# Kernel tuning notes

Measured on AMD Instinct MI355X. Metric: run time of the kernel, lower is better.

Reference implementation:

```python
import jax, jax.numpy as jnp
import numpy as np

N, IN_DIM, HIDDEN, OUT_DIM = 16384, 4, 64, 2


def setup_inputs() -> dict:
    key = jax.random.key(0)
    ks = jax.random.split(key, 12)
    x = jax.random.normal(ks[0], (N, IN_DIM), dtype=jnp.float32)
    adj = jax.random.uniform(ks[1], (N, N), dtype=jnp.float32)
    adj = adj / jnp.sum(adj, axis=1, keepdims=True)  # row-normalised
    s = 0.1
    return {
        "x": x,
        "adj": adj,
        # msg_mlp: Linear(4,64) -> Tanh -> Linear(64,64)
        "W1": jax.random.normal(ks[2], (IN_DIM, HIDDEN), dtype=jnp.float32) * s,
        "b1": jnp.zeros((HIDDEN,), dtype=jnp.float32),
        "W2": jax.random.normal(ks[3], (HIDDEN, HIDDEN), dtype=jnp.float32) * s,
        "b2": jnp.zeros((HIDDEN,), dtype=jnp.float32),
        # update_mlp: Linear(68,64) -> Tanh -> Linear(64,64) -> Tanh
        "U1": jax.random.normal(ks[4], (IN_DIM + HIDDEN, HIDDEN), dtype=jnp.float32) * s,
        "c1": jnp.zeros((HIDDEN,), dtype=jnp.float32),
        "U2": jax.random.normal(ks[5], (HIDDEN, HIDDEN), dtype=jnp.float32) * s,
        "c2": jnp.zeros((HIDDEN,), dtype=jnp.float32),
        # out_head: Linear(64,2)
        "Wo": jax.random.normal(ks[6], (HIDDEN, OUT_DIM), dtype=jnp.float32) * s,
        "bo": jnp.zeros((OUT_DIM,), dtype=jnp.float32),
    }


def reference(x, adj, W1, b1, W2, b2, U1, c1, U2, c2, Wo, bo):
    # messages = msg_mlp(x): (N, HIDDEN)
    messages = jnp.tanh(x @ W1 + b1) @ W2 + b2
    # aggregate over neighbours: (N,N) @ (N,HIDDEN)
    agg = adj @ messages
    # combined = [x, agg]: (N, IN_DIM+HIDDEN)
    combined = jnp.concatenate([x, agg], axis=-1)
    h = jnp.tanh(jnp.tanh(combined @ U1 + c1) @ U2 + c2)
    acc = h @ Wo + bo  # (N, OUT_DIM)
    return acc
```

## Files before the change

### kernel.cpp

```cpp
#include <hip/hip_runtime.h>
#include <math.h>

#define NN 16384
#define IN_DIM 4
#define HID 64
#define OUT_DIM 2
#define SPLITS 4
#define KCH (NN / SPLITS)

typedef __bf16 bf16x8 __attribute__((ext_vector_type(8)));
typedef float  f32x4  __attribute__((ext_vector_type(4)));

__global__ __launch_bounds__(256) void k_messages(
    const float* __restrict__ x, const float* __restrict__ W1,
    const float* __restrict__ b1, const float* __restrict__ W2,
    const float* __restrict__ b2, __bf16* __restrict__ msgT)
{
    __shared__ float  xs[64 * 4];
    __shared__ float  h1[64 * 64];
    __shared__ __bf16 mt[64 * 66];

    const int t = threadIdx.x;
    const int node0 = blockIdx.x * 64;
    xs[t] = x[node0 * 4 + t];
    __syncthreads();

    const int h = t & 63, g = t >> 6;
    for (int n = g * 16; n < g * 16 + 16; ++n) {
        float acc = b1[h];
        #pragma unroll
        for (int k = 0; k < 4; ++k) acc += xs[n * 4 + k] * W1[k * 64 + h];
        h1[n * 64 + h] = tanhf(acc);
    }
    __syncthreads();
    for (int n = g * 16; n < g * 16 + 16; ++n) {
        float acc = b2[h];
        #pragma unroll 8
        for (int k = 0; k < 64; ++k) acc += h1[n * 64 + k] * W2[k * 64 + h];
        mt[h * 66 + n] = (__bf16)acc;
    }
    __syncthreads();
    for (int slot = t; slot < 512; slot += 256) {
        const int r = slot >> 3, c = (slot & 7) * 8;
        bf16x8 v;
        #pragma unroll
        for (int j = 0; j < 8; ++j) v[j] = mt[r * 66 + c + j];
        *(bf16x8*)(msgT + (size_t)r * NN + node0 + c) = v;
    }
}

__global__ __launch_bounds__(256) void k_agg(
    const float* __restrict__ adj, const __bf16* __restrict__ msgT,
    float* __restrict__ part)
{
    const int t = threadIdx.x;
    const int wave = t >> 6, lane = t & 63;
    const int s = blockIdx.x >> 8;
    const int rowblk = blockIdx.x & 255;
    const int m0 = rowblk * 64 + wave * 16;
    const int c = lane & 15;
    const int kg = lane >> 4;

    const float*  ap = adj  + (size_t)(m0 + c) * NN + s * KCH + kg * 8;
    const __bf16* bp = msgT + (size_t)c * NN        + s * KCH + kg * 8;

    f32x4 acc0 = {}, acc1 = {}, acc2 = {}, acc3 = {};

    #pragma unroll 2
    for (int kk = 0; kk < KCH / 32; ++kk) {
        f32x4 a0 = *(const f32x4*)(ap);
        f32x4 a1 = *(const f32x4*)(ap + 4);
        ap += 32;
        bf16x8 b0v = *(const bf16x8*)(bp);
        bf16x8 b1v = *(const bf16x8*)(bp + 16 * (size_t)NN);
        bf16x8 b2v = *(const bf16x8*)(bp + 32 * (size_t)NN);
        bf16x8 b3v = *(const bf16x8*)(bp + 48 * (size_t)NN);
        bp += 32;
        bf16x8 af;
        af[0] = (__bf16)a0[0]; af[1] = (__bf16)a0[1];
        af[2] = (__bf16)a0[2]; af[3] = (__bf16)a0[3];
        af[4] = (__bf16)a1[0]; af[5] = (__bf16)a1[1];
        af[6] = (__bf16)a1[2]; af[7] = (__bf16)a1[3];
        acc0 = __builtin_amdgcn_mfma_f32_16x16x32_bf16(af, b0v, acc0, 0, 0, 0);
        acc1 = __builtin_amdgcn_mfma_f32_16x16x32_bf16(af, b1v, acc1, 0, 0, 0);
        acc2 = __builtin_amdgcn_mfma_f32_16x16x32_bf16(af, b2v, acc2, 0, 0, 0);
        acc3 = __builtin_amdgcn_mfma_f32_16x16x32_bf16(af, b3v, acc3, 0, 0, 0);
    }

    float* pp = part + (size_t)s * NN * HID;
    const int rbase = m0 + (lane >> 4) * 4;
    const int cbase = lane & 15;
    f32x4 accs[4] = {acc0, acc1, acc2, acc3};
    #pragma unroll
    for (int tt = 0; tt < 4; ++tt) {
        #pragma unroll
        for (int j = 0; j < 4; ++j) {
            pp[(size_t)(rbase + j) * HID + tt * 16 + cbase] = accs[tt][j];
        }
    }
}

__global__ __launch_bounds__(256) void k_update(
    const float* __restrict__ x, const float* __restrict__ part,
    const float* __restrict__ U1, const float* __restrict__ c1,
    const float* __restrict__ U2, const float* __restrict__ c2,
    const float* __restrict__ Wo, const float* __restrict__ bo,
    float* __restrict__ out)
{
    __shared__ float comb[64 * 73];
    __shared__ float h1s[64 * 66];

    const int t = threadIdx.x, h = t & 63, g = t >> 6;
    const int node0 = blockIdx.x * 64;

    comb[(t >> 2) * 73 + (t & 3)] = x[node0 * 4 + t];
    const float* P0 = part;
    const float* P1 = part + (size_t)1 * NN * HID;
    const float* P2 = part + (size_t)2 * NN * HID;
    const float* P3 = part + (size_t)3 * NN * HID;
    for (int n = g * 16; n < g * 16 + 16; ++n) {
        const size_t idx = (size_t)(node0 + n) * HID + h;
        comb[n * 73 + 4 + h] = P0[idx] + P1[idx] + P2[idx] + P3[idx];
    }
    __syncthreads();
    for (int n = g * 16; n < g * 16 + 16; ++n) {
        float acc = c1[h];
        #pragma unroll 4
        for (int k = 0; k < 68; ++k) acc += comb[n * 73 + k] * U1[k * 64 + h];
        h1s[n * 66 + h] = tanhf(acc);
    }
    __syncthreads();
    for (int n = g * 16; n < g * 16 + 16; ++n) {
        float acc = c2[h];
        #pragma unroll 8
        for (int k = 0; k < 64; ++k) acc += h1s[n * 66 + k] * U2[k * 64 + h];
        comb[n * 73 + h] = tanhf(acc);
    }
    __syncthreads();
    if (t < 128) {
        const int n = t >> 1, o = t & 1;
        float acc = bo[o];
        #pragma unroll 8
        for (int k = 0; k < 64; ++k) acc += comb[n * 73 + k] * Wo[k * 2 + o];
        out[(size_t)(node0 + n) * 2 + o] = acc;
    }
}

extern "C" void kernel_launch(void* const* d_in, const int* in_sizes, int n_in,
                              void* d_out, int out_size, void* d_ws, size_t ws_size,
                              hipStream_t stream)
{
    const float* x   = (const float*)d_in[0];
    const float* adj = (const float*)d_in[1];
    const float* W1  = (const float*)d_in[2];
    const float* b1  = (const float*)d_in[3];
    const float* W2  = (const float*)d_in[4];
    const float* b2  = (const float*)d_in[5];
    const float* U1  = (const float*)d_in[6];
    const float* c1  = (const float*)d_in[7];
    const float* U2  = (const float*)d_in[8];
    const float* c2  = (const float*)d_in[9];
    const float* Wo  = (const float*)d_in[10];
    const float* bo  = (const float*)d_in[11];
    float* out = (float*)d_out;

    __bf16* msgT = (__bf16*)d_ws;
    float*  part = (float*)((char*)d_ws + (size_t)HID * NN * sizeof(__bf16));

    k_messages<<<NN / 64, 256, 0, stream>>>(x, W1, b1, W2, b2, msgT);
    k_agg<<<256 * SPLITS, 256, 0, stream>>>(adj, msgT, part);
    k_update<<<NN / 64, 256, 0, stream>>>(x, part, U1, c1, U2, c2, Wo, bo, out);
}
```

Before: 414.7 us.

## Stage adjacency tiles into LDS via async global_load_lds with double buffering

The aggregation kernel no longer has each lane load scattered 32-byte pieces of adjacency rows straight into registers. It streams 64x64 fp32 tiles of adj into LDS with async global-to-LDS 16-byte loads, which gives 256-byte contiguous row segments per 16 lanes. Loads are double-buffered so the next tile is in flight while MFMAs consume the current one, and an XOR swizzle avoids LDS bank conflicts on the fragment reads. The aim is better coalescing and overlap on the bandwidth-bound adj stream, at the cost of 32 KB of LDS per block and a barrier per tile.

```diff
diff --git a/kernel.cpp b/kernel.cpp
--- a/kernel.cpp
+++ b/kernel.cpp
@@ -7,9 +7,17 @@
 #define OUT_DIM 2
 #define SPLITS 4
 #define KCH (NN / SPLITS)
+#define BK 64
+#define NT (KCH / BK)
 
 typedef __bf16 bf16x8 __attribute__((ext_vector_type(8)));
 typedef float  f32x4  __attribute__((ext_vector_type(4)));
+
+__device__ __forceinline__ void gload_lds16(const float* g, void* lds) {
+    __builtin_amdgcn_global_load_lds(
+        (const __attribute__((address_space(1))) void*)g,
+        (__attribute__((address_space(3))) void*)lds, 16, 0, 0);
+}
 
 __global__ __launch_bounds__(256) void k_messages(
     const float* __restrict__ x, const float* __restrict__ W1,
@@ -53,49 +61,77 @@
     const float* __restrict__ adj, const __bf16* __restrict__ msgT,
     float* __restrict__ part)
 {
+    __shared__ float As[2][64 * 64];
+
     const int t = threadIdx.x;
     const int wave = t >> 6, lane = t & 63;
     const int s = blockIdx.x >> 8;
     const int rowblk = blockIdx.x & 255;
-    const int m0 = rowblk * 64 + wave * 16;
-    const int c = lane & 15;
-    const int kg = lane >> 4;
-
-    const float*  ap = adj  + (size_t)(m0 + c) * NN + s * KCH + kg * 8;
-    const __bf16* bp = msgT + (size_t)c * NN        + s * KCH + kg * 8;
+    const int m0 = rowblk * 64;
+    const int k0 = s * KCH;
+
+    const int trow = t >> 4;
+    const int tcol = t & 15;
+    const int cchunk = tcol ^ trow;
+    const float* src0 = adj + (size_t)(m0 + trow) * NN + k0 + cchunk * 4;
+    const size_t rstep = (size_t)16 * NN;
+
+    const int r15 = lane & 15;
+    const int kg  = lane >> 4;
+    const int arow = wave * 16 + r15;
+    const __bf16* bp = msgT + (size_t)r15 * NN + k0 + kg * 8;
 
     f32x4 acc0 = {}, acc1 = {}, acc2 = {}, acc3 = {};
 
-    #pragma unroll 2
-    for (int kk = 0; kk < KCH / 32; ++kk) {
-        f32x4 a0 = *(const f32x4*)(ap);
-        f32x4 a1 = *(const f32x4*)(ap + 4);
-        ap += 32;
-        bf16x8 b0v = *(const bf16x8*)(bp);
-        bf16x8 b1v = *(const bf16x8*)(bp + 16 * (size_t)NN);
-        bf16x8 b2v = *(const bf16x8*)(bp + 32 * (size_t)NN);
-        bf16x8 b3v = *(const bf16x8*)(bp + 48 * (size_t)NN);
-        bp += 32;
-        bf16x8 af;
-        af[0] = (__bf16)a0[0]; af[1] = (__bf16)a0[1];
-        af[2] = (__bf16)a0[2]; af[3] = (__bf16)a0[3];
-        af[4] = (__bf16)a1[0]; af[5] = (__bf16)a1[1];
-        af[6] = (__bf16)a1[2]; af[7] = (__bf16)a1[3];
-        acc0 = __builtin_amdgcn_mfma_f32_16x16x32_bf16(af, b0v, acc0, 0, 0, 0);
-        acc1 = __builtin_amdgcn_mfma_f32_16x16x32_bf16(af, b1v, acc1, 0, 0, 0);
-        acc2 = __builtin_amdgcn_mfma_f32_16x16x32_bf16(af, b2v, acc2, 0, 0, 0);
-        acc3 = __builtin_amdgcn_mfma_f32_16x16x32_bf16(af, b3v, acc3, 0, 0, 0);
+    #pragma unroll
+    for (int r = 0; r < 4; ++r)
+        gload_lds16(src0 + (size_t)r * rstep,
+                    (char*)&As[0][0] + r * 4096 + wave * 1024);
+    asm volatile("s_waitcnt vmcnt(0)" ::: "memory");
+    __syncthreads();
+
+    int cur = 0;
+    for (int kt = 0; kt < NT; ++kt) {
+        if (kt + 1 < NT) {
+            const float* snext = src0 + (size_t)(kt + 1) * BK;
+            #pragma unroll
+            for (int r = 0; r < 4; ++r)
+                gload_lds16(snext + (size_t)r * rstep,
+                            (char*)&As[cur ^ 1][0] + r * 4096 + wave * 1024);
+        }
+
+        const char* Ab = (const char*)&As[cur][0] + arow * 256;
+        const __bf16* bkp = bp + (size_t)kt * BK;
+        #pragma unroll
+        for (int kk = 0; kk < 2; ++kk) {
+            f32x4 alo = *(const f32x4*)(Ab + (((kk * 8 + kg * 2 + 0) ^ r15) * 16));
+            f32x4 ahi = *(const f32x4*)(Ab + (((kk * 8 + kg * 2 + 1) ^ r15) * 16));
+            bf16x8 af;
+            af[0] = (__bf16)alo[0]; af[1] = (__bf16)alo[1];
+            af[2] = (__bf16)alo[2]; af[3] = (__bf16)alo[3];
+            af[4] = (__bf16)ahi[0]; af[5] = (__bf16)ahi[1];
+            af[6] = (__bf16)ahi[2]; af[7] = (__bf16)ahi[3];
+            bf16x8 b0v = *(const bf16x8*)(bkp + kk * 32);
+            bf16x8 b1v = *(const bf16x8*)(bkp + kk * 32 + 16 * (size_t)NN);
+            bf16x8 b2v = *(const bf16x8*)(bkp + kk * 32 + 32 * (size_t)NN);
+            bf16x8 b3v = *(const bf16x8*)(bkp + kk * 32 + 48 * (size_t)NN);
+            acc0 = __builtin_amdgcn_mfma_f32_16x16x32_bf16(af, b0v, acc0, 0, 0, 0);
+            acc1 = __builtin_amdgcn_mfma_f32_16x16x32_bf16(af, b1v, acc1, 0, 0, 0);
+            acc2 = __builtin_amdgcn_mfma_f32_16x16x32_bf16(af, b2v, acc2, 0, 0, 0);
+            acc3 = __builtin_amdgcn_mfma_f32_16x16x32_bf16(af, b3v, acc3, 0, 0, 0);
+        }
+        __syncthreads();
+        cur ^= 1;
     }
 
     float* pp = part + (size_t)s * NN * HID;
-    const int rbase = m0 + (lane >> 4) * 4;
-    const int cbase = lane & 15;
+    const int rbase = m0 + wave * 16 + kg * 4;
     f32x4 accs[4] = {acc0, acc1, acc2, acc3};
     #pragma unroll
     for (int tt = 0; tt < 4; ++tt) {
         #pragma unroll
         for (int j = 0; j < 4; ++j) {
-            pp[(size_t)(rbase + j) * HID + tt * 16 + cbase] = accs[tt][j];
+            pp[(size_t)(rbase + j) * HID + tt * 16 + r15] = accs[tt][j];
         }
     }
 }
```

After: 357.5 us. 13.8% less time.

## Stream adjacency through double-buffered LDS via async global_load_lds, drop split-K

Applied to the files above, without the earlier changes.

The aggregation kernel now stages each wave's 16 adjacency rows into a double-buffered, XOR-swizzled LDS tile with async global-to-LDS loads, and prefetches the message operands one step ahead so HBM streaming overlaps the MFMA work. The split-K partial sums are removed: each 128-thread block covers the full K range for 32 rows, so the update kernel reads a single aggregate instead of four partials. This cuts partial-sum traffic and aims to keep more loads in flight, at the cost of fewer waves per CU, longer per-block serial loops, and hand-tuned vmcnt waits that must match the issue pattern.

```diff
diff --git a/kernel.cpp b/kernel.cpp
--- a/kernel.cpp
+++ b/kernel.cpp
@@ -5,11 +5,22 @@
 #define IN_DIM 4
 #define HID 64
 #define OUT_DIM 2
-#define SPLITS 4
-#define KCH (NN / SPLITS)
+#define BK 256
+#define NT (NN / BK)
 
 typedef __bf16 bf16x8 __attribute__((ext_vector_type(8)));
 typedef float  f32x4  __attribute__((ext_vector_type(4)));
+
+__device__ __forceinline__ void gload_lds16(const float* g, void* lds) {
+    __builtin_amdgcn_global_load_lds(
+        (const __attribute__((address_space(1))) void*)g,
+        (__attribute__((address_space(3))) void*)lds, 16, 0, 0);
+}
+
+template<int N> __device__ __forceinline__ void waitv() {
+    asm volatile("s_waitcnt vmcnt(%0)" :: "n"(N) : "memory");
+    __builtin_amdgcn_sched_barrier(0);
+}
 
 __global__ __launch_bounds__(256) void k_messages(
     const float* __restrict__ x, const float* __restrict__ W1,
@@ -49,59 +60,100 @@
     }
 }
 
-__global__ __launch_bounds__(256) void k_agg(
+__global__ __launch_bounds__(128, 1) void k_agg(
     const float* __restrict__ adj, const __bf16* __restrict__ msgT,
-    float* __restrict__ part)
-{
+    float* __restrict__ agg)
+{
+    __shared__ float As[2][2][16 * BK];
+
     const int t = threadIdx.x;
     const int wave = t >> 6, lane = t & 63;
-    const int s = blockIdx.x >> 8;
-    const int rowblk = blockIdx.x & 255;
-    const int m0 = rowblk * 64 + wave * 16;
-    const int c = lane & 15;
-    const int kg = lane >> 4;
-
-    const float*  ap = adj  + (size_t)(m0 + c) * NN + s * KCH + kg * 8;
-    const __bf16* bp = msgT + (size_t)c * NN        + s * KCH + kg * 8;
+    const int m0 = blockIdx.x * 32 + wave * 16;
+    const int r15 = lane & 15;
+    const int kg  = lane >> 4;
+
+    const float*  arow  = adj  + (size_t)m0 * NN;
+    const __bf16* bbase = msgT + (size_t)r15 * NN + kg * 8;
+
+    float* wbuf0 = &As[0][wave][0];
+    float* wbuf1 = &As[1][wave][0];
 
     f32x4 acc0 = {}, acc1 = {}, acc2 = {}, acc3 = {};
-
-    #pragma unroll 2
-    for (int kk = 0; kk < KCH / 32; ++kk) {
-        f32x4 a0 = *(const f32x4*)(ap);
-        f32x4 a1 = *(const f32x4*)(ap + 4);
-        ap += 32;
-        bf16x8 b0v = *(const bf16x8*)(bp);
-        bf16x8 b1v = *(const bf16x8*)(bp + 16 * (size_t)NN);
-        bf16x8 b2v = *(const bf16x8*)(bp + 32 * (size_t)NN);
-        bf16x8 b3v = *(const bf16x8*)(bp + 48 * (size_t)NN);
-        bp += 32;
-        bf16x8 af;
-        af[0] = (__bf16)a0[0]; af[1] = (__bf16)a0[1];
-        af[2] = (__bf16)a0[2]; af[3] = (__bf16)a0[3];
-        af[4] = (__bf16)a1[0]; af[5] = (__bf16)a1[1];
-        af[6] = (__bf16)a1[2]; af[7] = (__bf16)a1[3];
-        acc0 = __builtin_amdgcn_mfma_f32_16x16x32_bf16(af, b0v, acc0, 0, 0, 0);
-        acc1 = __builtin_amdgcn_mfma_f32_16x16x32_bf16(af, b1v, acc1, 0, 0, 0);
-        acc2 = __builtin_amdgcn_mfma_f32_16x16x32_bf16(af, b2v, acc2, 0, 0, 0);
-        acc3 = __builtin_amdgcn_mfma_f32_16x16x32_bf16(af, b3v, acc3, 0, 0, 0);
-    }
-
-    float* pp = part + (size_t)s * NN * HID;
-    const int rbase = m0 + (lane >> 4) * 4;
-    const int cbase = lane & 15;
+    bf16x8 bc0, bc1, bc2, bc3, bn0, bn1, bn2, bn3;
+
+    #pragma unroll
+    for (int g = 0; g < 16; ++g)
+        gload_lds16(arow + (size_t)g * NN + ((lane ^ g) << 2), wbuf0 + g * BK);
+    bc0 = *(const bf16x8*)(bbase);
+    bc1 = *(const bf16x8*)(bbase + 16 * (size_t)NN);
+    bc2 = *(const bf16x8*)(bbase + 32 * (size_t)NN);
+    bc3 = *(const bf16x8*)(bbase + 48 * (size_t)NN);
+
+#define KSTEP(KT, KK, WAITN, DOSTAGE, DOBN)                                        \
+    {                                                                              \
+        if (DOBN) {                                                                \
+            const int nkt = ((KK) == 7) ? (KT) + 1 : (KT);                         \
+            const int nkk = ((KK) + 1) & 7;                                        \
+            const __bf16* bp = bbase + (size_t)nkt * BK + nkk * 32;                \
+            bn0 = *(const bf16x8*)(bp);                                            \
+            bn1 = *(const bf16x8*)(bp + 16 * (size_t)NN);                          \
+            bn2 = *(const bf16x8*)(bp + 32 * (size_t)NN);                          \
+            bn3 = *(const bf16x8*)(bp + 48 * (size_t)NN);                          \
+        }                                                                          \
+        if (WAITN) waitv<(WAITN) ? (WAITN) : 63>();                                \
+        const float* Ab = (((KT) & 1) ? wbuf1 : wbuf0) + r15 * BK;                 \
+        f32x4 alo = *(const f32x4*)(Ab + ((((KK) * 8 + kg * 2 + 0) ^ r15) << 2));  \
+        f32x4 ahi = *(const f32x4*)(Ab + ((((KK) * 8 + kg * 2 + 1) ^ r15) << 2));  \
+        bf16x8 af;                                                                 \
+        af[0] = (__bf16)alo[0]; af[1] = (__bf16)alo[1];                            \
+        af[2] = (__bf16)alo[2]; af[3] = (__bf16)alo[3];                            \
+        af[4] = (__bf16)ahi[0]; af[5] = (__bf16)ahi[1];                            \
+        af[6] = (__bf16)ahi[2]; af[7] = (__bf16)ahi[3];                            \
+        acc0 = __builtin_amdgcn_mfma_f32_16x16x32_bf16(af, bc0, acc0, 0, 0, 0);    \
+        acc1 = __builtin_amdgcn_mfma_f32_16x16x32_bf16(af, bc1, acc1, 0, 0, 0);    \
+        acc2 = __builtin_amdgcn_mfma_f32_16x16x32_bf16(af, bc2, acc2, 0, 0, 0);    \
+        acc3 = __builtin_amdgcn_mfma_f32_16x16x32_bf16(af, bc3, acc3, 0, 0, 0);    \
+        if (DOSTAGE) {                                                             \
+            float* dst = (((KT) & 1) ? wbuf0 : wbuf1);                             \
+            _Pragma("unroll")                                                      \
+            for (int q = 0; q < 4; ++q) {                                          \
+                const int g = (KK) * 4 + q;                                        \
+                gload_lds16(arow + (size_t)g * NN + (size_t)((KT) + 1) * BK        \
+                                 + ((lane ^ g) << 2), dst + g * BK);               \
+            }                                                                      \
+        }                                                                          \
+        bc0 = bn0; bc1 = bn1; bc2 = bn2; bc3 = bn3;                                \
+        __builtin_amdgcn_sched_barrier(0);                                         \
+    }
+
+    KSTEP(0, 0, 8, 1, 1);
+    #pragma unroll
+    for (int kk = 1; kk < 8; ++kk) KSTEP(0, kk, 0, (kk < 4), 1);
+
+    for (int kt = 1; kt < NT - 1; ++kt) {
+        KSTEP(kt, 0, 20, 1, 1);
+        #pragma unroll
+        for (int kk = 1; kk < 8; ++kk) KSTEP(kt, kk, 0, (kk < 4), 1);
+    }
+
+    KSTEP((NT - 1), 0, 20, 0, 1);
+    #pragma unroll
+    for (int kk = 1; kk < 8; ++kk) KSTEP((NT - 1), kk, 0, 0, (kk != 7));
+#undef KSTEP
+
+    const int rb = m0 + kg * 4;
     f32x4 accs[4] = {acc0, acc1, acc2, acc3};
     #pragma unroll
     for (int tt = 0; tt < 4; ++tt) {
         #pragma unroll
         for (int j = 0; j < 4; ++j) {
-            pp[(size_t)(rbase + j) * HID + tt * 16 + cbase] = accs[tt][j];
+            agg[(size_t)(rb + j) * HID + tt * 16 + r15] = accs[tt][j];
         }
     }
 }
 
 __global__ __launch_bounds__(256) void k_update(
-    const float* __restrict__ x, const float* __restrict__ part,
+    const float* __restrict__ x, const float* __restrict__ agg,
     const float* __restrict__ U1, const float* __restrict__ c1,
     const float* __restrict__ U2, const float* __restrict__ c2,
     const float* __restrict__ Wo, const float* __restrict__ bo,
@@ -114,13 +166,8 @@
     const int node0 = blockIdx.x * 64;
 
     comb[(t >> 2) * 73 + (t & 3)] = x[node0 * 4 + t];
-    const float* P0 = part;
-    const float* P1 = part + (size_t)1 * NN * HID;
-    const float* P2 = part + (size_t)2 * NN * HID;
-    const float* P3 = part + (size_t)3 * NN * HID;
-    for (int n = g * 16; n < g * 16 + 16; ++n) {
-        const size_t idx = (size_t)(node0 + n) * HID + h;
-        comb[n * 73 + 4 + h] = P0[idx] + P1[idx] + P2[idx] + P3[idx];
+    for (int n = g * 16; n < g * 16 + 16; ++n) {
+        comb[n * 73 + 4 + h] = agg[(size_t)(node0 + n) * HID + h];
     }
     __syncthreads();
     for (int n = g * 16; n < g * 16 + 16; ++n) {
@@ -165,9 +212,9 @@
     float* out = (float*)d_out;
 
     __bf16* msgT = (__bf16*)d_ws;
-    float*  part = (float*)((char*)d_ws + (size_t)HID * NN * sizeof(__bf16));
+    float*  agg  = (float*)((char*)d_ws + (size_t)HID * NN * sizeof(__bf16));
 
     k_messages<<<NN / 64, 256, 0, stream>>>(x, W1, b1, W2, b2, msgT);
-    k_agg<<<256 * SPLITS, 256, 0, stream>>>(adj, msgT, part);
-    k_update<<<NN / 64, 256, 0, stream>>>(x, part, U1, c1, U2, c2, Wo, bo, out);
-}
+    k_agg<<<NN / 32, 128, 0, stream>>>(adj, msgT, agg);
+    k_update<<<NN / 64, 256, 0, stream>>>(x, agg, U1, c1, U2, c2, Wo, bo, out);
+}
```

Measured after the change: 373.1 us. 1.11x faster.
